# Performance work log

Measured on AMD Instinct MI355X. Metric: run time of the kernel, lower is better.

The kernel has to match this reference:

```python
import jax, jax.numpy as jnp
import numpy as np

H = 10  # hidden size per direction
I = 1   # input size


def _lstm_scan(x_tbi, Wih, Whh, bih, bhh):
    """Single-direction LSTM over time-major input x_tbi: [T, B, I] -> [T, B, H].
    PyTorch gate order: i, f, g, o."""
    T, B, _ = x_tbi.shape
    # Precompute input contribution for all timesteps: [T, B, 4H]
    pre = jnp.einsum('tbi,gi->tbg', x_tbi, Wih) + bih + bhh

    def step(carry, p):
        h, c = carry
        gates = p + h @ Whh.T  # [B, 4H]
        i, f, g, o = jnp.split(gates, 4, axis=-1)
        i = jax.nn.sigmoid(i)
        f = jax.nn.sigmoid(f)
        g = jnp.tanh(g)
        o = jax.nn.sigmoid(o)
        c = f * c + i * g
        h = o * jnp.tanh(c)
        return (h, c), h

    h0 = jnp.zeros((B, H), x_tbi.dtype)
    (_, _), hs = jax.lax.scan(step, (h0, h0), pre)
    return hs  # [T, B, H]


def setup_inputs() -> dict:
    key = jax.random.key(0)
    ks = jax.random.split(key, 12)
    B, T = 256, 4096
    s = 1.0 / np.sqrt(H)  # PyTorch LSTM init range
    u = lambda k, shape: jax.random.uniform(k, shape, jnp.float32, -s, s)
    inp = {
        'data': jax.random.normal(ks[0], (B, T, I), jnp.float32),
        # forward direction
        'Wih_f': u(ks[1], (4 * H, I)),
        'Whh_f': u(ks[2], (4 * H, H)),
        'bih_f': u(ks[3], (4 * H,)),
        'bhh_f': u(ks[4], (4 * H,)),
        # backward direction
        'Wih_b': u(ks[5], (4 * H, I)),
        'Whh_b': u(ks[6], (4 * H, H)),
        'bih_b': u(ks[7], (4 * H,)),
        'bhh_b': u(ks[8], (4 * H,)),
        # final linear (kaiming_uniform fan_in=20 -> bound sqrt(6/20))
        'Wout': jax.random.uniform(ks[9], (1, 2 * H), jnp.float32, -np.sqrt(6.0 / (2 * H)), np.sqrt(6.0 / (2 * H))),
        'bout': jax.random.uniform(ks[10], (1,), jnp.float32, -1.0 / np.sqrt(2 * H), 1.0 / np.sqrt(2 * H)),
    }
    return inp


def reference(data, Wih_f, Whh_f, bih_f, bhh_f, Wih_b, Whh_b, bih_b, bhh_b, Wout, bout):
    # data: [B, T, 1] (batch_first) -> time-major [T, B, 1]
    x = jnp.transpose(data, (1, 0, 2))
    hf = _lstm_scan(x, Wih_f, Whh_f, bih_f, bhh_f)                 # [T, B, H]
    hb = _lstm_scan(x[::-1], Wih_b, Whh_b, bih_b, bhh_b)[::-1]     # [T, B, H]
    h = jnp.concatenate([hf, hb], axis=-1)                          # [T, B, 2H]
    y = h @ Wout.T + bout                                           # [T, B, 1]
    return jnp.transpose(y, (1, 0, 2))                              # [B, T, 1]
```

## Files before the change

kernel.cpp:

```cpp
#include <hip/hip_runtime.h>

#define T_LEN 4096
#define B_N   256
#define SEG_N 8
#define OWN   512
#define WARM  128
#define SMAX  (OWN + WARM)
#define YSTR  (SMAX + 2)
#define L2E   1.4426950408889634f

typedef float v2f __attribute__((ext_vector_type(2)));

__device__ __forceinline__ v2f pk_mul(v2f a, v2f b) {
    v2f d; asm("v_pk_mul_f32 %0, %1, %2" : "=v"(d) : "v"(a), "v"(b)); return d;
}
__device__ __forceinline__ v2f pk_fma(v2f a, v2f b, v2f c) {
    v2f d; asm("v_pk_fma_f32 %0, %1, %2, %3" : "=v"(d) : "v"(a), "v"(b), "v"(c)); return d;
}

template <int S>
__device__ __forceinline__ float ror16(float v) {
    if constexpr (S == 0) return v;
    else return __int_as_float(__builtin_amdgcn_update_dpp(
        0, __float_as_int(v), 0x120 | S, 0xF, 0xF, true));
}

template <int DIR>
__device__ __forceinline__ void scan_dir(
    const float* __restrict__ data,
    const float* __restrict__ Wih, const float* __restrict__ Whh,
    const float* __restrict__ bih, const float* __restrict__ bhh,
    const float* __restrict__ Wout, const float* __restrict__ bout,
    float* __restrict__ out, float* __restrict__ ylds, int seg, int b0)
{
    const int l = threadIdx.x;
    const int c = l >> 4;
    const int u = l & 15;

    v2f WI[8], WF[8], WG[8], WO[8];
    v2f WX_if = {0.f, 0.f}, WX_go = {0.f, 0.f};
    v2f B_if  = {0.f, 0.f}, B_go  = {0.f, 0.f};

    if (u < 10) {
        const int rI = u, rF = 10 + u, rG = 20 + u, rO = 30 + u;
#pragma unroll
        for (int s = 0; s < 8; ++s) {
            const int mA = (u - s) & 15, mB = (u - s - 8) & 15;
            const float aI = (mA < 10) ? -L2E * Whh[rI * 10 + mA] : 0.f;
            const float bI = (mB < 10) ? -L2E * Whh[rI * 10 + mB] : 0.f;
            const float aF = (mA < 10) ? -L2E * Whh[rF * 10 + mA] : 0.f;
            const float bF = (mB < 10) ? -L2E * Whh[rF * 10 + mB] : 0.f;
            const float aG = (mA < 10) ? 2.f * L2E * Whh[rG * 10 + mA] : 0.f;
            const float bG = (mB < 10) ? 2.f * L2E * Whh[rG * 10 + mB] : 0.f;
            const float aO = (mA < 10) ? -L2E * Whh[rO * 10 + mA] : 0.f;
            const float bO = (mB < 10) ? -L2E * Whh[rO * 10 + mB] : 0.f;
            WI[s] = (v2f){aI, bI}; WF[s] = (v2f){aF, bF};
            WG[s] = (v2f){aG, bG}; WO[s] = (v2f){aO, bO};
        }
        WX_if = (v2f){-L2E * Wih[rI], -L2E * Wih[rF]};
        WX_go = (v2f){2.f * L2E * Wih[rG], -L2E * Wih[rO]};
        B_if = (v2f){-L2E * (bih[rI] + bhh[rI]), -L2E * (bih[rF] + bhh[rF])};
        B_go = (v2f){2.f * L2E * (bih[rG] + bhh[rG]), -L2E * (bih[rO] + bhh[rO])};
    } else if (u == 10) {
#pragma unroll
        for (int s = 0; s < 8; ++s) {
            const int mA = (u - s) & 15, mB = (u - s - 8) & 15;
            WI[s] = (v2f){(mA < 10) ? Wout[DIR * 10 + mA] : 0.f,
                          (mB < 10) ? Wout[DIR * 10 + mB] : 0.f};
            WF[s] = (v2f){0.f, 0.f}; WG[s] = (v2f){0.f, 0.f}; WO[s] = (v2f){0.f, 0.f};
        }
        B_if = (v2f){(DIR == 0) ? bout[0] : 0.f, 0.f};
    } else {
#pragma unroll
        for (int s = 0; s < 8; ++s) {
            WI[s] = (v2f){0.f, 0.f}; WF[s] = (v2f){0.f, 0.f};
            WG[s] = (v2f){0.f, 0.f}; WO[s] = (v2f){0.f, 0.f};
        }
    }

    const int wpre  = (DIR == 0) ? ((seg == 0) ? 0 : WARM)
                                 : ((seg == SEG_N - 1) ? 0 : WARM);
    const int steps = OWN + wpre;
    const int t0 = seg * OWN - wpre;
    const int t1 = seg * OWN + OWN - 1 + wpre;

    int yi = (u == 10) ? (c * YSTR) : (4 * YSTR + l);
    const int ywd = (u == 10) ? 1 : 0;

    float h = 0.0f, C = 0.0f;

    const float* xrow = data + (size_t)(b0 + c) * T_LEN;
    const float* px = (DIR == 0) ? (xrow + t0) : (xrow + t1 - 7);
    const int pstep = (DIR == 0) ? 8 : -8;
    float4 A  = *(const float4*)px;
    float4 Bv = *(const float4*)(px + 4);

#define H2BUILD                                                               \
    v2f h2[8];                                                                \
    h2[0] = (v2f){h,           ror16<8>(h)};                                  \
    h2[1] = (v2f){ror16<1>(h), ror16<9>(h)};                                  \
    h2[2] = (v2f){ror16<2>(h), ror16<10>(h)};                                 \
    h2[3] = (v2f){ror16<3>(h), ror16<11>(h)};                                 \
    h2[4] = (v2f){ror16<4>(h), ror16<12>(h)};                                 \
    h2[5] = (v2f){ror16<5>(h), ror16<13>(h)};                                 \
    h2[6] = (v2f){ror16<6>(h), ror16<14>(h)};                                 \
    h2[7] = (v2f){ror16<7>(h), ror16<15>(h)};

#define STEP(XV)                                                              \
    {                                                                         \
        const v2f X2 = {XV, XV};                                              \
        const v2f pif = pk_fma(X2, WX_if, B_if);                              \
        const v2f pgo = pk_fma(X2, WX_go, B_go);                              \
        H2BUILD                                                               \
        v2f ai = pk_mul(h2[0], WI[0]);                                        \
        v2f af = pk_mul(h2[0], WF[0]);                                        \
        v2f ag = pk_mul(h2[0], WG[0]);                                        \
        v2f ao = pk_mul(h2[0], WO[0]);                                        \
        _Pragma("unroll")                                                     \
        for (int s = 1; s < 8; ++s) {                                         \
            ai = pk_fma(h2[s], WI[s], ai);                                    \
            af = pk_fma(h2[s], WF[s], af);                                    \
            ag = pk_fma(h2[s], WG[s], ag);                                    \
            ao = pk_fma(h2[s], WO[s], ao);                                    \
        }                                                                     \
        const float gi = (ai.x + ai.y) + pif.x;                               \
        const float gf = (af.x + af.y) + pif.y;                               \
        const float gg = (ag.x + ag.y) + pgo.x;                               \
        const float go_ = (ao.x + ao.y) + pgo.y;                              \
        ylds[yi] = gi;  yi += ywd;         \
        const float ri = __builtin_amdgcn_rcpf(1.f + __builtin_amdgcn_exp2f(gi)); \
        const float rf = __builtin_amdgcn_rcpf(1.f + __builtin_amdgcn_exp2f(gf)); \
        const float rg = __builtin_amdgcn_rcpf(1.f + __builtin_amdgcn_exp2f(gg)); \
        const float ro = __builtin_amdgcn_rcpf(1.f + __builtin_amdgcn_exp2f(go_)); \
        const float aiv = (2.f * L2E) * ri;                                   \
        const float agv = fmaf(-2.f, rg, 1.f);                                \
        C = fmaf(rf, C, aiv * agv);                       \
        const float r2 = __builtin_amdgcn_rcpf(1.f + __builtin_amdgcn_exp2f(C)); \
        const float mo = -2.f * ro;                                           \
        h = fmaf(mo, r2, ro);                            \
    }

    const int nch = steps >> 3;
    for (int it = 0; it < nch; ++it) {
        const float* pn = px + ((it + 1 < nch) ? (it + 1) : it) * pstep;
        float4 An = *(const float4*)pn;
        float4 Bn = *(const float4*)(pn + 4);
        const float xs[8] = {A.x, A.y, A.z, A.w, Bv.x, Bv.y, Bv.z, Bv.w};
#pragma unroll
        for (int r = 0; r < 8; ++r) {
            const float xv = xs[(DIR == 0) ? r : (7 - r)];
            STEP(xv)
        }
        A = An; Bv = Bn;
    }

    {
        H2BUILD
        v2f ai = pk_mul(h2[0], WI[0]);
#pragma unroll
        for (int s = 1; s < 8; ++s) ai = pk_fma(h2[s], WI[s], ai);
        ylds[yi] = (ai.x + ai.y) + B_if.x;
    }

    for (int i = l; i < 4 * OWN; i += 64) {
        const int ci = i >> 9;
        const int io = i & (OWN - 1);
        const int t  = seg * OWN + io;
        const int sp = (DIR == 0) ? (wpre + io) : (OWN - 1 + wpre - io);
        atomicAdd(&out[(size_t)(b0 + ci) * T_LEN + t], ylds[ci * YSTR + sp + 1]);
    }
#undef STEP
#undef H2BUILD
}

__global__ __launch_bounds__(64) void Model_82008105550530_kernel(
    const float* __restrict__ data,
    const float* __restrict__ Wih_f, const float* __restrict__ Whh_f,
    const float* __restrict__ bih_f, const float* __restrict__ bhh_f,
    const float* __restrict__ Wih_b, const float* __restrict__ Whh_b,
    const float* __restrict__ bih_b, const float* __restrict__ bhh_b,
    const float* __restrict__ Wout, const float* __restrict__ bout,
    float* __restrict__ out)
{
    __shared__ float ylds[4 * YSTR + 64];
    const int b0  = (blockIdx.x & 63) << 2;
    const int grp = blockIdx.x >> 6;
    const int seg = grp & 7;
    if ((grp >> 3) == 0)
        scan_dir<0>(data, Wih_f, Whh_f, bih_f, bhh_f, Wout, bout, out, ylds, seg, b0);
    else
        scan_dir<1>(data, Wih_b, Whh_b, bih_b, bhh_b, Wout, bout, out, ylds, seg, b0);
}

extern "C" void kernel_launch(void* const* d_in, const int* in_sizes, int n_in,
                              void* d_out, int out_size, void* d_ws, size_t ws_size,
                              hipStream_t stream) {
    const float* data  = (const float*)d_in[0];
    const float* Wih_f = (const float*)d_in[1];
    const float* Whh_f = (const float*)d_in[2];
    const float* bih_f = (const float*)d_in[3];
    const float* bhh_f = (const float*)d_in[4];
    const float* Wih_b = (const float*)d_in[5];
    const float* Whh_b = (const float*)d_in[6];
    const float* bih_b = (const float*)d_in[7];
    const float* bhh_b = (const float*)d_in[8];
    const float* Wout  = (const float*)d_in[9];
    const float* bout  = (const float*)d_in[10];
    float* out = (float*)d_out;

    hipMemsetAsync(out, 0, (size_t)out_size * sizeof(float), stream);
    Model_82008105550530_kernel<<<1024, 64, 0, stream>>>(
        data, Wih_f, Whh_f, bih_f, bhh_f, Wih_b, Whh_b, bih_b, bhh_b, Wout, bout, out);
}
```

Before: 136.4 us.

## Remap LSTM lanes to gate-per-lane with 16 batches per wave and shorter segments

```diff
diff --git a/kernel.cpp b/kernel.cpp
--- a/kernel.cpp
+++ b/kernel.cpp
@@ -2,8 +2,8 @@
 
 #define T_LEN 4096
 #define B_N   256
-#define SEG_N 8
-#define OWN   512
+#define SEG_N 32
+#define OWN   128
 #define WARM  128
 #define SMAX  (OWN + WARM)
 #define YSTR  (SMAX + 2)
@@ -18,11 +18,14 @@
     v2f d; asm("v_pk_fma_f32 %0, %1, %2, %3" : "=v"(d) : "v"(a), "v"(b), "v"(c)); return d;
 }
 
-template <int S>
-__device__ __forceinline__ float ror16(float v) {
-    if constexpr (S == 0) return v;
-    else return __int_as_float(__builtin_amdgcn_update_dpp(
-        0, __float_as_int(v), 0x120 | S, 0xF, 0xF, true));
+template <int CTRL>
+__device__ __forceinline__ float dpp_qp(float v) {
+    return __int_as_float(__builtin_amdgcn_update_dpp(
+        0, __float_as_int(v), CTRL, 0xF, 0xF, true));
+}
+
+__device__ __forceinline__ float sig_core(float a) {
+    return __builtin_amdgcn_rcpf(1.0f + __builtin_amdgcn_exp2f(a));
 }
 
 template <int DIR>
@@ -34,49 +37,30 @@
     float* __restrict__ out, float* __restrict__ ylds, int seg, int b0)
 {
     const int l = threadIdx.x;
-    const int c = l >> 4;
-    const int u = l & 15;
-
-    v2f WI[8], WF[8], WG[8], WO[8];
-    v2f WX_if = {0.f, 0.f}, WX_go = {0.f, 0.f};
-    v2f B_if  = {0.f, 0.f}, B_go  = {0.f, 0.f};
-
-    if (u < 10) {
-        const int rI = u, rF = 10 + u, rG = 20 + u, rO = 30 + u;
-#pragma unroll
-        for (int s = 0; s < 8; ++s) {
-            const int mA = (u - s) & 15, mB = (u - s - 8) & 15;
-            const float aI = (mA < 10) ? -L2E * Whh[rI * 10 + mA] : 0.f;
-            const float bI = (mB < 10) ? -L2E * Whh[rI * 10 + mB] : 0.f;
-            const float aF = (mA < 10) ? -L2E * Whh[rF * 10 + mA] : 0.f;
-            const float bF = (mB < 10) ? -L2E * Whh[rF * 10 + mB] : 0.f;
-            const float aG = (mA < 10) ? 2.f * L2E * Whh[rG * 10 + mA] : 0.f;
-            const float bG = (mB < 10) ? 2.f * L2E * Whh[rG * 10 + mB] : 0.f;
-            const float aO = (mA < 10) ? -L2E * Whh[rO * 10 + mA] : 0.f;
-            const float bO = (mB < 10) ? -L2E * Whh[rO * 10 + mB] : 0.f;
-            WI[s] = (v2f){aI, bI}; WF[s] = (v2f){aF, bF};
-            WG[s] = (v2f){aG, bG}; WO[s] = (v2f){aO, bO};
-        }
-        WX_if = (v2f){-L2E * Wih[rI], -L2E * Wih[rF]};
-        WX_go = (v2f){2.f * L2E * Wih[rG], -L2E * Wih[rO]};
-        B_if = (v2f){-L2E * (bih[rI] + bhh[rI]), -L2E * (bih[rF] + bhh[rF])};
-        B_go = (v2f){2.f * L2E * (bih[rG] + bhh[rG]), -L2E * (bih[rO] + bhh[rO])};
-    } else if (u == 10) {
-#pragma unroll
-        for (int s = 0; s < 8; ++s) {
-            const int mA = (u - s) & 15, mB = (u - s - 8) & 15;
-            WI[s] = (v2f){(mA < 10) ? Wout[DIR * 10 + mA] : 0.f,
-                          (mB < 10) ? Wout[DIR * 10 + mB] : 0.f};
-            WF[s] = (v2f){0.f, 0.f}; WG[s] = (v2f){0.f, 0.f}; WO[s] = (v2f){0.f, 0.f};
-        }
-        B_if = (v2f){(DIR == 0) ? bout[0] : 0.f, 0.f};
-    } else {
-#pragma unroll
-        for (int s = 0; s < 8; ++s) {
-            WI[s] = (v2f){0.f, 0.f}; WF[s] = (v2f){0.f, 0.f};
-            WG[s] = (v2f){0.f, 0.f}; WO[s] = (v2f){0.f, 0.f};
-        }
-    }
+    const int q = l >> 2;
+    const int k = l & 3;
+
+    const float sc = (k == 2) ? (2.0f * L2E) : (-L2E);
+    const float aa = (k == 0) ? (2.0f * L2E) : ((k == 2) ? -2.0f : 1.0f);
+    const float bb = (k == 2) ? 1.0f : 0.0f;
+
+    v2f W2[50], wih2[5], b2[5], wout2[5];
+#pragma unroll
+    for (int j = 0; j < 10; ++j) {
+        const int row = k * 10 + j;
+#pragma unroll
+        for (int m = 0; m < 5; ++m)
+            W2[j * 5 + m] = (v2f){sc * Whh[row * 10 + 2 * m],
+                                  sc * Whh[row * 10 + 2 * m + 1]};
+    }
+#pragma unroll
+    for (int m = 0; m < 5; ++m) {
+        const int rA = k * 10 + 2 * m, rB = rA + 1;
+        wih2[m] = (v2f){sc * Wih[rA], sc * Wih[rB]};
+        b2[m]   = (v2f){sc * (bih[rA] + bhh[rA]), sc * (bih[rB] + bhh[rB])};
+        wout2[m] = (v2f){Wout[DIR * 10 + 2 * m], Wout[DIR * 10 + 2 * m + 1]};
+    }
+    const float ybias = (DIR == 0) ? bout[0] : 0.0f;
 
     const int wpre  = (DIR == 0) ? ((seg == 0) ? 0 : WARM)
                                  : ((seg == SEG_N - 1) ? 0 : WARM);
@@ -84,60 +68,74 @@
     const int t0 = seg * OWN - wpre;
     const int t1 = seg * OWN + OWN - 1 + wpre;
 
-    int yi = (u == 10) ? (c * YSTR) : (4 * YSTR + l);
-    const int ywd = (u == 10) ? 1 : 0;
-
-    float h = 0.0f, C = 0.0f;
-
-    const float* xrow = data + (size_t)(b0 + c) * T_LEN;
+    int yi = (k == 0) ? (q * YSTR) : (16 * YSTR + l);
+    const int ywd = (k == 0) ? 1 : 0;
+
+    v2f hb2[5];
+    float cx[5], cy[5];
+#pragma unroll
+    for (int m = 0; m < 5; ++m) {
+        hb2[m] = (v2f){0.f, 0.f}; cx[m] = 0.f; cy[m] = 0.f;
+    }
+
+    const float* xrow = data + (size_t)(b0 + q) * T_LEN;
     const float* px = (DIR == 0) ? (xrow + t0) : (xrow + t1 - 7);
     const int pstep = (DIR == 0) ? 8 : -8;
     float4 A  = *(const float4*)px;
     float4 Bv = *(const float4*)(px + 4);
 
-#define H2BUILD                                                               \
-    v2f h2[8];                                                                \
-    h2[0] = (v2f){h,           ror16<8>(h)};                                  \
-    h2[1] = (v2f){ror16<1>(h), ror16<9>(h)};                                  \
-    h2[2] = (v2f){ror16<2>(h), ror16<10>(h)};                                 \
-    h2[3] = (v2f){ror16<3>(h), ror16<11>(h)};                                 \
-    h2[4] = (v2f){ror16<4>(h), ror16<12>(h)};                                 \
-    h2[5] = (v2f){ror16<5>(h), ror16<13>(h)};                                 \
-    h2[6] = (v2f){ror16<6>(h), ror16<14>(h)};                                 \
-    h2[7] = (v2f){ror16<7>(h), ror16<15>(h)};
+#define YDOT(BIAS)                                                            \
+    {                                                                         \
+        v2f sy = pk_fma(wout2[0], hb2[0], (v2f){BIAS, 0.f});                  \
+        sy = pk_fma(wout2[1], hb2[1], sy);                                    \
+        sy = pk_fma(wout2[2], hb2[2], sy);                                    \
+        sy = pk_fma(wout2[3], hb2[3], sy);                                    \
+        sy = pk_fma(wout2[4], hb2[4], sy);                                    \
+        ylds[yi] = sy.x + sy.y;  yi += ywd;                                   \
+    }
 
 #define STEP(XV)                                                              \
     {                                                                         \
         const v2f X2 = {XV, XV};                                              \
-        const v2f pif = pk_fma(X2, WX_if, B_if);                              \
-        const v2f pgo = pk_fma(X2, WX_go, B_go);                              \
-        H2BUILD                                                               \
-        v2f ai = pk_mul(h2[0], WI[0]);                                        \
-        v2f af = pk_mul(h2[0], WF[0]);                                        \
-        v2f ag = pk_mul(h2[0], WG[0]);                                        \
-        v2f ao = pk_mul(h2[0], WO[0]);                                        \
-        _Pragma("unroll")                                                     \
-        for (int s = 1; s < 8; ++s) {                                         \
-            ai = pk_fma(h2[s], WI[s], ai);                                    \
-            af = pk_fma(h2[s], WF[s], af);                                    \
-            ag = pk_fma(h2[s], WG[s], ag);                                    \
-            ao = pk_fma(h2[s], WO[s], ao);                                    \
+        v2f pre2[5];                                                          \
+        _Pragma("unroll")                                                     \
+        for (int m = 0; m < 5; ++m) pre2[m] = pk_fma(X2, wih2[m], b2[m]);     \
+        float acc[10];                                                        \
+        _Pragma("unroll")                                                     \
+        for (int j = 0; j < 10; ++j) {                                        \
+            const float pj = (j & 1) ? pre2[j >> 1].y : pre2[j >> 1].x;       \
+            v2f s = pk_fma(W2[j * 5 + 0], hb2[0], (v2f){pj, 0.f});            \
+            s = pk_fma(W2[j * 5 + 1], hb2[1], s);                             \
+            s = pk_fma(W2[j * 5 + 2], hb2[2], s);                             \
+            s = pk_fma(W2[j * 5 + 3], hb2[3], s);                             \
+            s = pk_fma(W2[j * 5 + 4], hb2[4], s);                             \
+            acc[j] = s.x + s.y;                                               \
         }                                                                     \
-        const float gi = (ai.x + ai.y) + pif.x;                               \
-        const float gf = (af.x + af.y) + pif.y;                               \
-        const float gg = (ag.x + ag.y) + pgo.x;                               \
-        const float go_ = (ao.x + ao.y) + pgo.y;                              \
-        ylds[yi] = gi;  yi += ywd;         \
-        const float ri = __builtin_amdgcn_rcpf(1.f + __builtin_amdgcn_exp2f(gi)); \
-        const float rf = __builtin_amdgcn_rcpf(1.f + __builtin_amdgcn_exp2f(gf)); \
-        const float rg = __builtin_amdgcn_rcpf(1.f + __builtin_amdgcn_exp2f(gg)); \
-        const float ro = __builtin_amdgcn_rcpf(1.f + __builtin_amdgcn_exp2f(go_)); \
-        const float aiv = (2.f * L2E) * ri;                                   \
-        const float agv = fmaf(-2.f, rg, 1.f);                                \
-        C = fmaf(rf, C, aiv * agv);                       \
-        const float r2 = __builtin_amdgcn_rcpf(1.f + __builtin_amdgcn_exp2f(C)); \
-        const float mo = -2.f * ro;                                           \
-        h = fmaf(mo, r2, ro);                            \
+        YDOT(ybias)                                \
+                \
+        float actx[5], acty[5];                                               \
+        _Pragma("unroll")                                                     \
+        for (int m = 0; m < 5; ++m) {                                         \
+            actx[m] = fmaf(aa, sig_core(acc[2 * m]), bb);                     \
+            acty[m] = fmaf(aa, sig_core(acc[2 * m + 1]), bb);                 \
+        }                                                                     \
+        _Pragma("unroll")                                                     \
+        for (int m = 0; m < 5; ++m) {                                         \
+            const float f1x = dpp_qp<0xB1>(actx[m]);          \
+            const float f1y = dpp_qp<0xB1>(acty[m]);                          \
+            const float g2x = dpp_qp<0x4E>(actx[m]);          \
+            const float g2y = dpp_qp<0x4E>(acty[m]);                          \
+            const float o3x = dpp_qp<0x1B>(actx[m]);          \
+            const float o3y = dpp_qp<0x1B>(acty[m]);                          \
+            cx[m] = fmaf(f1x, cx[m], actx[m] * g2x);     \
+            cy[m] = fmaf(f1y, cy[m], acty[m] * g2y);                          \
+            const float thx = fmaf(-2.f, sig_core(cx[m]), 1.f);               \
+            const float thy = fmaf(-2.f, sig_core(cy[m]), 1.f);               \
+            const float hnx = o3x * thx;         \
+            const float hny = o3y * thy;                                      \
+            hb2[m].x = dpp_qp<0x00>(hnx);      \
+            hb2[m].y = dpp_qp<0x00>(hny);                                     \
+        }                                                                     \
     }
 
     const int nch = steps >> 3;
@@ -154,26 +152,20 @@
         A = An; Bv = Bn;
     }
 
-    {
-        H2BUILD
-        v2f ai = pk_mul(h2[0], WI[0]);
-#pragma unroll
-        for (int s = 1; s < 8; ++s) ai = pk_fma(h2[s], WI[s], ai);
-        ylds[yi] = (ai.x + ai.y) + B_if.x;
-    }
-
-    for (int i = l; i < 4 * OWN; i += 64) {
-        const int ci = i >> 9;
+    YDOT(ybias)
+
+    for (int i = l; i < 16 * OWN; i += 64) {
+        const int ci = i >> 7;
         const int io = i & (OWN - 1);
         const int t  = seg * OWN + io;
         const int sp = (DIR == 0) ? (wpre + io) : (OWN - 1 + wpre - io);
         atomicAdd(&out[(size_t)(b0 + ci) * T_LEN + t], ylds[ci * YSTR + sp + 1]);
     }
 #undef STEP
-#undef H2BUILD
-}
-
-__global__ __launch_bounds__(64) void Model_82008105550530_kernel(
+#undef YDOT
+}
+
+__global__ __launch_bounds__(64, 1) void Model_82008105550530_kernel(
     const float* __restrict__ data,
     const float* __restrict__ Wih_f, const float* __restrict__ Whh_f,
     const float* __restrict__ bih_f, const float* __restrict__ bhh_f,
@@ -182,11 +174,12 @@
     const float* __restrict__ Wout, const float* __restrict__ bout,
     float* __restrict__ out)
 {
-    __shared__ float ylds[4 * YSTR + 64];
-    const int b0  = (blockIdx.x & 63) << 2;
-    const int grp = blockIdx.x >> 6;
-    const int seg = grp & 7;
-    if ((grp >> 3) == 0)
+    __shared__ float ylds[16 * YSTR + 64];
+    const int bid = blockIdx.x;
+    const int dir = bid >> 9;
+    const int seg = (bid >> 4) & 31;
+    const int b0  = (bid & 15) << 4;
+    if (dir == 0)
         scan_dir<0>(data, Wih_f, Whh_f, bih_f, bhh_f, Wout, bout, out, ylds, seg, b0);
     else
         scan_dir<1>(data, Wih_b, Whh_b, bih_b, bhh_b, Wout, bout, out, ylds, seg, b0);
```

Measured after the change: 145.2 us. 6.5% more time.
